# Performance work log

Hardware: AMD Instinct MI355X
Metric: run time of the kernel (lower is better)

Reference implementation:

```python
import jax, jax.numpy as jnp
import numpy as np

N_NODES = 10000
N_EDGES = 160000
B = 128
HEADS = 4
DIMS = [36, 128, 256, 512]
NEG_SLOPE = 0.2  # PyG GATConv default


def setup_inputs() -> dict:
    key = jax.random.key(0)
    ks = jax.random.split(key, 32)
    inp = {}
    inp["x"] = jax.random.normal(ks[0], (N_NODES, DIMS[0]), jnp.float32)
    inp["edge_index"] = jax.random.randint(ks[1], (2, N_EDGES), 0, N_NODES)
    inp["batch"] = jnp.sort(jax.random.randint(ks[2], (N_NODES,), 0, B))
    ki = 3
    for i in range(3):
        din, dout = DIMS[i], DIMS[i + 1]
        C = dout // HEADS
        inp[f"gcn_w{i}"] = jax.random.normal(ks[ki], (din, dout), jnp.float32) * (din ** -0.5); ki += 1
        inp[f"gcn_b{i}"] = jnp.zeros((dout,), jnp.float32)
        inp[f"gat_w{i}"] = jax.random.normal(ks[ki], (dout, dout), jnp.float32) * (dout ** -0.5); ki += 1
        inp[f"gat_as{i}"] = jax.random.normal(ks[ki], (HEADS, C), jnp.float32) * 0.1; ki += 1
        inp[f"gat_ad{i}"] = jax.random.normal(ks[ki], (HEADS, C), jnp.float32) * 0.1; ki += 1
        inp[f"gat_b{i}"] = jnp.zeros((dout,), jnp.float32)
    D = DIMS[-1]
    inp["ap_w1"] = jax.random.normal(ks[ki], (D, D // 2), jnp.float32) * (D ** -0.5); ki += 1
    inp["ap_b1"] = jnp.zeros((D // 2,), jnp.float32)
    inp["ap_w2"] = jax.random.normal(ks[ki], (D // 2, 1), jnp.float32) * ((D // 2) ** -0.5); ki += 1
    inp["ap_b2"] = jnp.zeros((1,), jnp.float32)
    return inp


def _gcn(x, w, b, src, dst, n):
    # PyG GCNConv: add self-loops, symmetric deg^-1/2 normalization, bias after agg
    h = x @ w  # [N, dout]
    deg = jax.ops.segment_sum(jnp.ones_like(dst, dtype=h.dtype), dst, n) + 1.0  # incl. self-loop
    dinv = deg ** -0.5
    norm = dinv[src] * dinv[dst]  # [E]
    agg = jax.ops.segment_sum(h[src] * norm[:, None], dst, n)
    agg = agg + h * (dinv * dinv)[:, None]  # self-loop messages
    return agg + b


def _gat(x, w, a_s, a_d, b, src, dst, n):
    # PyG GATConv: self-loops, leaky-relu logits, segment softmax over dst, concat heads
    C = w.shape[1] // HEADS
    h = (x @ w).reshape(n, HEADS, C)
    alpha_src = (h * a_s).sum(-1)  # [N, H]
    alpha_dst = (h * a_d).sum(-1)  # [N, H]
    loop = jnp.arange(n)
    s = jnp.concatenate([src, loop])
    d = jnp.concatenate([dst, loop])
    e = jax.nn.leaky_relu(alpha_src[s] + alpha_dst[d], NEG_SLOPE)  # [E+N, H]
    m = jax.ops.segment_max(e, d, n)
    ex = jnp.exp(e - m[d])
    den = jax.ops.segment_sum(ex, d, n)
    alpha = ex / den[d]  # [E+N, H]
    out = jax.ops.segment_sum(h[s] * alpha[:, :, None], d, n)  # [N, H, C]
    return out.reshape(n, HEADS * C) + b


def _forward(x, edge_index, batch, params, ap_w1, ap_b1, ap_w2, ap_b2):
    src, dst = edge_index[0], edge_index[1]
    n = x.shape[0]
    x_in = x
    n_layers = len(params)
    for i, (gw, gb, aw, a_s, a_d, ab) in enumerate(params):
        h = jax.nn.relu(_gcn(x, gw, gb, src, dst, n))  # dropout is identity in eval
        x = h + _gat(h, aw, a_s, a_d, ab, src, dst, n)
        if i < n_layers - 1:
            if x.shape[-1] == x_in.shape[-1]:
                x = x + x_in
            x_in = x
    # attention pooling (global softmax then per-graph masked renorm)
    a = jnp.tanh(x @ ap_w1 + ap_b1) @ ap_w2 + ap_b2  # [N, 1]
    a = jax.nn.softmax(a, axis=0)
    mask = jax.nn.one_hot(batch, B, dtype=x.dtype)  # [N, B]
    aw_ = a * mask
    aw_ = aw_ / (aw_.sum(0, keepdims=True) + 1e-8)
    graph_emb = aw_.T @ x  # [B, D]
    cnt = jax.ops.segment_sum(jnp.ones((n,), x.dtype), batch, B)
    ssum = jax.ops.segment_sum(x, batch, B)
    mean = ssum / jnp.maximum(cnt, 1.0)[:, None]
    smax = jax.ops.segment_max(x, batch, B)
    return jnp.concatenate([graph_emb, mean, smax, ssum], axis=1)  # [B, 4*D]


def reference(x, edge_index, batch,
              gcn_w0, gcn_b0, gat_w0, gat_as0, gat_ad0, gat_b0,
              gcn_w1, gcn_b1, gat_w1, gat_as1, gat_ad1, gat_b1,
              gcn_w2, gcn_b2, gat_w2, gat_as2, gat_ad2, gat_b2,
              ap_w1, ap_b1, ap_w2, ap_b2):
    params = [
        (gcn_w0, gcn_b0, gat_w0, gat_as0, gat_ad0, gat_b0),
        (gcn_w1, gcn_b1, gat_w1, gat_as1, gat_ad1, gat_b1),
        (gcn_w2, gcn_b2, gat_w2, gat_as2, gat_ad2, gat_b2),
    ]
    return _forward(x, edge_index, batch, params, ap_w1, ap_b1, ap_w2, ap_b2)
```

## Files before the change

### kernel.cpp

```cpp
#include <hip/hip_runtime.h>
#include <math.h>

#define NN 10000
#define NE 160000
#define NB 128
#define NH 4
#define DOUT 512
#define NEG 0.2f
#define CNT_BLKS ((NE + 255) / 256)

typedef __attribute__((ext_vector_type(8))) short short8;
typedef __attribute__((ext_vector_type(4))) float f32x4;
typedef __attribute__((ext_vector_type(4))) unsigned short us4;

__device__ __forceinline__ float leakyf(float v){ return fmaxf(v, NEG*v); }
__device__ __forceinline__ void fma4(float4& a, const float4 v, float w){
  a.x += v.x*w; a.y += v.y*w; a.z += v.z*w; a.w += v.w*w;
}
__device__ __forceinline__ unsigned short f2bf(float f){
  unsigned int u = __float_as_uint(f);
  u += 0x7FFFu + ((u >> 16) & 1u);
  return (unsigned short)(u >> 16);
}
__device__ __forceinline__ float bf2f(unsigned short h){
  return __uint_as_float(((unsigned int)h) << 16);
}
__device__ __forceinline__ void split2(float v, unsigned short& h, unsigned short& l){
  h = f2bf(v);
  l = f2bf(v - bf2f(h));
}
__device__ __forceinline__ void store_hl(unsigned short* H, unsigned short* L,
                                         size_t base, float4 v){
  us4 h, l; unsigned short hh, ll;
  split2(v.x, hh, ll); h[0]=hh; l[0]=ll;
  split2(v.y, hh, ll); h[1]=hh; l[1]=ll;
  split2(v.z, hh, ll); h[2]=hh; l[2]=ll;
  split2(v.w, hh, ll); h[3]=hh; l[3]=ll;
  *(us4*)&H[base] = h;
  *(us4*)&L[base] = l;
}
__device__ __forceinline__ void gl_lds16(const unsigned short* g, unsigned short* l){
  __builtin_amdgcn_global_load_lds(
      (const __attribute__((address_space(1))) unsigned int*)g,
      (__attribute__((address_space(3))) unsigned int*)l, 16, 0, 0);
}

struct AllConv {
  const float* src[7];
  unsigned short* dh[7];
  unsigned short* dl[7];
  int K[7], Mm[7], Kp[7], tot[7];
};

__global__ void k_count_conv(const int* __restrict__ dst, int* __restrict__ cnt,
                             AllConv a, int convTot){
  int bid = blockIdx.x;
  if (bid < CNT_BLKS){
    int e = bid*256 + threadIdx.x;
    if (e < NE) atomicAdd(&cnt[dst[e]], 1);
  } else {
    int idx = (bid - CNT_BLKS)*256 + threadIdx.x;
    if (idx >= convTot) return;
    int j = 0;
    while (idx >= a.tot[j]){ idx -= a.tot[j]; j++; }
    int Kp = a.Kp[j], K = a.K[j], M = a.Mm[j];
    int kk = idx % Kp, m = idx / Kp;
    float v = (kk < K) ? a.src[j][(size_t)kk*M + m] : 0.f;
    unsigned short h, l; split2(v, h, l);
    a.dh[j][idx] = h; a.dl[j][idx] = l;
  }
}

__global__ __launch_bounds__(1024) void k_scan_all(
    const int* __restrict__ cnt, const int* __restrict__ batch,
    int* __restrict__ rowptr, float* __restrict__ dinv,
    int* __restrict__ cursor, float* __restrict__ apre,
    int* __restrict__ starts, int* __restrict__ perm){
  __shared__ int sh[NN];
  __shared__ int pref[1024];
  __shared__ int hist[512];
  __shared__ int hbase[512];
  int t = threadIdx.x;
  for (int i = t; i < NN; i += 1024) sh[i] = cnt[i];
  if (t < 512) hist[t] = 0;
  if (t <= NB){
    int lo = 0, hi = NN;
    while (lo < hi){ int mid = (lo + hi) >> 1; if (batch[mid] < t) lo = mid + 1; else hi = mid; }
    starts[t] = lo;
  }
  __syncthreads();
  int base = t*10;
  int csum = 0;
#pragma unroll
  for (int k = 0; k < 10; k++){
    int i = base + k;
    if (i < NN){
      csum += sh[i];
      atomicAdd(&hist[511 - min(sh[i], 511)], 1);
    }
  }
  pref[t] = csum; __syncthreads();
  int horig = (t < 512) ? hist[t] : 0;
  for (int o = 1; o < 1024; o <<= 1){
    int v = (t >= o) ? pref[t - o] : 0;
    __syncthreads();
    pref[t] += v;
    __syncthreads();
  }
  for (int o = 1; o < 512; o <<= 1){
    int v = 0;
    if (t < 512 && t >= o) v = hist[t - o];
    __syncthreads();
    if (t < 512 && t >= o) hist[t] += v;
    __syncthreads();
  }
  if (t < 512) hbase[t] = hist[t] - horig;
  __syncthreads();
  int run = pref[t] - csum;
#pragma unroll
  for (int k = 0; k < 10; k++){
    int i = base + k;
    if (i < NN){
      int c = sh[i];
      rowptr[i] = run;
      run += c;
      dinv[i] = rsqrtf((float)c + 1.f);
      cursor[i] = 0;
      apre[i] = 0.f;
      int pos = atomicAdd(&hbase[511 - min(c, 511)], 1);
      perm[pos] = i;
    }
  }
  if (t == 1023) rowptr[NN] = pref[1023];
}

__global__ void k_fill(const int* __restrict__ src, const int* __restrict__ dst,
                       const int* __restrict__ rowptr, int* __restrict__ cursor,
                       int* __restrict__ colidx){
  int e = blockIdx.x*blockDim.x + threadIdx.x;
  if (e >= NE) return;
  int d = dst[e];
  int pos = atomicAdd(&cursor[d], 1);
  colidx[rowptr[d] + pos] = src[e];
}

#define GBM 64
#define GBN 128
#define GBK 64
__global__ __launch_bounds__(256) void k_gemm_bf3(
    const unsigned short* __restrict__ Ah, const unsigned short* __restrict__ Al,
    const unsigned short* __restrict__ Bh, const unsigned short* __restrict__ Bl,
    float* __restrict__ C, int N, int Kp, int M, int mode,
    const float* __restrict__ bias, unsigned short* __restrict__ outH,
    unsigned short* __restrict__ outL,
    const float* __restrict__ a_s, const float* __restrict__ a_d,
    float* __restrict__ as_o, float* __restrict__ ad_o, int Cdim){
  __shared__ unsigned short AsH[2*GBM*32], AsL[2*GBM*32];
  __shared__ unsigned short BsH[2*GBN*32], BsL[2*GBN*32];
  __shared__ float sred[2][GBM][4];
  int gx = M / GBN;
  int gy = (N + GBM - 1) / GBM;
  const int G = 8;
  int bid = blockIdx.x;
  int full = gy / G;
  int bid_full = full * G * gx;
  int by, bx;
  if (bid < bid_full){
    int g = bid / (G*gx); int rem = bid % (G*gx);
    by = g*G + rem % G; bx = rem / G;
  } else {
    int rem = bid - bid_full; int rows = gy - full*G;
    by = full*G + rem % rows; bx = rem / rows;
  }
  int row0 = by * GBM, col0 = bx * GBN;
  int t = threadIdx.x;
  int w = t >> 6, L = t & 63;
  int lm = L & 15, lq = L >> 4;
  int wc = w * 32;

  int sr = L >> 2, sc = L & 3;
  int art = w*16 + sr;
  int ga  = (sc - ((art >> 1) & 3)) & 3;
  int agrow = min(row0 + art, N-1);
  int brt0 = w*16 + sr;
  int brt1 = (w+4)*16 + sr;
  int gb0 = (sc - ((brt0 >> 1) & 3)) & 3;
  int gb1 = (sc - ((brt1 >> 1) & 3)) & 3;
  int bgrow0 = col0 + brt0, bgrow1 = col0 + brt1;

  int rc = (lq + (lm >> 1)) & 3;
  int aoff[4], boff[2];
#pragma unroll
  for (int mi = 0; mi < 4; mi++) aoff[mi] = (mi*16 + lm)*32 + rc*8;
#pragma unroll
  for (int ni = 0; ni < 2; ni++) boff[ni] = (wc + ni*16 + lm)*32 + rc*8;

  f32x4 acc[4][2];
#pragma unroll
  for (int i = 0; i < 4; i++)
#pragma unroll
    for (int j = 0; j < 2; j++) acc[i][j] = (f32x4){0.f,0.f,0.f,0.f};

  int nk = Kp / GBK;
  for (int kt = 0; kt < nk; kt++){
    int k0 = kt * GBK;
    if (kt) __syncthreads();
#pragma unroll
    for (int h = 0; h < 2; h++){
      int kh = k0 + h*32;
      gl_lds16(&Ah[(size_t)agrow*Kp + kh + ga*8],  &AsH[h*2048 + w*512]);
      gl_lds16(&Al[(size_t)agrow*Kp + kh + ga*8],  &AsL[h*2048 + w*512]);
      gl_lds16(&Bh[(size_t)bgrow0*Kp + kh + gb0*8], &BsH[h*4096 + w*512]);
      gl_lds16(&Bh[(size_t)bgrow1*Kp + kh + gb1*8], &BsH[h*4096 + (w+4)*512]);
      gl_lds16(&Bl[(size_t)bgrow0*Kp + kh + gb0*8], &BsL[h*4096 + w*512]);
      gl_lds16(&Bl[(size_t)bgrow1*Kp + kh + gb1*8], &BsL[h*4096 + (w+4)*512]);
    }
    __syncthreads();

#pragma unroll
    for (int h = 0; h < 2; h++){
      short8 ah[4], al[4], bh[2], bl[2];
#pragma unroll
      for (int mi = 0; mi < 4; mi++){
        ah[mi] = *(const short8*)&AsH[h*2048 + aoff[mi]];
        al[mi] = *(const short8*)&AsL[h*2048 + aoff[mi]];
      }
#pragma unroll
      for (int ni = 0; ni < 2; ni++){
        bh[ni] = *(const short8*)&BsH[h*4096 + boff[ni]];
        bl[ni] = *(const short8*)&BsL[h*4096 + boff[ni]];
      }
#pragma unroll
      for (int mi = 0; mi < 4; mi++)
#pragma unroll
        for (int ni = 0; ni < 2; ni++){
          acc[mi][ni] = __builtin_amdgcn_mfma_f32_16x16x32_bf16(ah[mi], bh[ni], acc[mi][ni], 0, 0, 0);
          acc[mi][ni] = __builtin_amdgcn_mfma_f32_16x16x32_bf16(ah[mi], bl[ni], acc[mi][ni], 0, 0, 0);
          acc[mi][ni] = __builtin_amdgcn_mfma_f32_16x16x32_bf16(al[mi], bh[ni], acc[mi][ni], 0, 0, 0);
        }
    }
  }
  if (mode == 1){
#pragma unroll
    for (int mi = 0; mi < 4; mi++)
#pragma unroll
      for (int ni = 0; ni < 2; ni++){
#pragma unroll
        for (int r = 0; r < 4; r++){
          int row = row0 + mi*16 + lq*4 + r;
          int col = col0 + wc + ni*16 + lm;
          if (row < N){
            float v = fmaxf(acc[mi][ni][r] + bias[col], 0.f);
            unsigned short hh, ll; split2(v, hh, ll);
            outH[(size_t)row*M + col] = hh;
            outL[(size_t)row*M + col] = ll;
            C[(size_t)row*M + col] = v;
          }
        }
      }
  } else if (mode != 3){
#pragma unroll
    for (int mi = 0; mi < 4; mi++)
#pragma unroll
      for (int ni = 0; ni < 2; ni++){
#pragma unroll
        for (int r = 0; r < 4; r++){
          int row = row0 + mi*16 + lq*4 + r;
          int col = col0 + wc + ni*16 + lm;
          if (row < N) C[(size_t)row*M + col] = acc[mi][ni][r];
        }
      }
  }
  if (mode == 2){
    float sA0 = a_s[col0 + wc + lm], sA1 = a_s[col0 + wc + 16 + lm];
    float dA0 = a_d[col0 + wc + lm], dA1 = a_d[col0 + wc + 16 + lm];
#pragma unroll
    for (int mi = 0; mi < 4; mi++)
#pragma unroll
      for (int r = 0; r < 4; r++){
        float vs = acc[mi][0][r]*sA0 + acc[mi][1][r]*sA1;
        float vd = acc[mi][0][r]*dA0 + acc[mi][1][r]*dA1;
#pragma unroll
        for (int o = 1; o <= 8; o <<= 1){
          vs += __shfl_xor(vs, o);
          vd += __shfl_xor(vd, o);
        }
        if (lm == 0){
          int row = mi*16 + lq*4 + r;
          sred[0][row][w] = vs;
          sred[1][row][w] = vd;
        }
      }
    __syncthreads();
    if (t < GBM){
      int n = row0 + t;
      if (n < N){
        int wph = Cdim >> 5;
        int nheads = 4 / wph;
        for (int g = 0; g < nheads; g++){
          float ss = 0.f, dd = 0.f;
          for (int q = 0; q < wph; q++){
            ss += sred[0][t][g*wph + q];
            dd += sred[1][t][g*wph + q];
          }
          int hd = (col0 + g*wph*32) / Cdim;
          as_o[n*NH + hd] = ss;
          ad_o[n*NH + hd] = dd;
        }
      }
    }
  } else if (mode == 3){
    float b0 = bias[col0 + wc + lm], b1v = bias[col0 + wc + 16 + lm];
    float w0v = a_s[col0 + wc + lm], w1v = a_s[col0 + wc + 16 + lm];
#pragma unroll
    for (int mi = 0; mi < 4; mi++)
#pragma unroll
      for (int r = 0; r < 4; r++){
        float v = tanhf(acc[mi][0][r] + b0)*w0v + tanhf(acc[mi][1][r] + b1v)*w1v;
#pragma unroll
        for (int o = 1; o <= 8; o <<= 1) v += __shfl_xor(v, o);
        if (lm == 0) sred[0][mi*16 + lq*4 + r][w] = v;
      }
    __syncthreads();
    if (t < GBM){
      int n = row0 + t;
      if (n < N){
        float s = sred[0][t][0] + sred[0][t][1] + sred[0][t][2] + sred[0][t][3];
        atomicAdd(&as_o[n], s);
      }
    }
  }
}

__global__ __launch_bounds__(256) void k_gcn_pre0(
    const float* __restrict__ x0, const float* __restrict__ dinv,
    const int* __restrict__ rowptr, const int* __restrict__ colidx,
    const int* __restrict__ perm,
    unsigned short* __restrict__ outH, unsigned short* __restrict__ outL){
  int t = threadIdx.x;
  int sub = t & 15;
  int gid = blockIdx.x*16 + (t >> 4);
  if (gid >= NN) return;
  int n = perm[gid];
  int f0 = sub*4;
  bool act = f0 < 36;
  int b = rowptr[n], e = rowptr[n+1];
  float dn = dinv[n];
  float4 a0 = make_float4(0,0,0,0), a1 = make_float4(0,0,0,0);
  float4 a2 = make_float4(0,0,0,0), a3 = make_float4(0,0,0,0);
  if (act){
    float4 sv = *(const float4*)&x0[(size_t)n*36 + f0];
    int j = b;
    for (; j + 7 < e; j += 8){
      int s0 = colidx[j],   s1 = colidx[j+1], s2 = colidx[j+2], s3 = colidx[j+3];
      int s4 = colidx[j+4], s5 = colidx[j+5], s6 = colidx[j+6], s7 = colidx[j+7];
      float w0 = dinv[s0], w1 = dinv[s1], w2 = dinv[s2], w3 = dinv[s3];
      float w4 = dinv[s4], w5 = dinv[s5], w6 = dinv[s6], w7 = dinv[s7];
      float4 v0 = *(const float4*)&x0[(size_t)s0*36 + f0];
      float4 v1 = *(const float4*)&x0[(size_t)s1*36 + f0];
      float4 v2 = *(const float4*)&x0[(size_t)s2*36 + f0];
      float4 v3 = *(const float4*)&x0[(size_t)s3*36 + f0];
      float4 v4 = *(const float4*)&x0[(size_t)s4*36 + f0];
      float4 v5 = *(const float4*)&x0[(size_t)s5*36 + f0];
      float4 v6 = *(const float4*)&x0[(size_t)s6*36 + f0];
      float4 v7 = *(const float4*)&x0[(size_t)s7*36 + f0];
      fma4(a0, v0, w0*dn); fma4(a1, v1, w1*dn);
      fma4(a2, v2, w2*dn); fma4(a3, v3, w3*dn);
      fma4(a0, v4, w4*dn); fma4(a1, v5, w5*dn);
      fma4(a2, v6, w6*dn); fma4(a3, v7, w7*dn);
    }
    for (; j + 3 < e; j += 4){
      int s0 = colidx[j], s1 = colidx[j+1], s2 = colidx[j+2], s3 = colidx[j+3];
      float w0 = dinv[s0], w1 = dinv[s1], w2 = dinv[s2], w3 = dinv[s3];
      float4 v0 = *(const float4*)&x0[(size_t)s0*36 + f0];
      float4 v1 = *(const float4*)&x0[(size_t)s1*36 + f0];
      float4 v2 = *(const float4*)&x0[(size_t)s2*36 + f0];
      float4 v3 = *(const float4*)&x0[(size_t)s3*36 + f0];
      fma4(a0, v0, w0*dn); fma4(a1, v1, w1*dn);
      fma4(a2, v2, w2*dn); fma4(a3, v3, w3*dn);
    }
    for (; j < e; j++){
      int s = colidx[j];
      float4 v = *(const float4*)&x0[(size_t)s*36 + f0];
      fma4(a0, v, dinv[s]*dn);
    }
    float4 acc = make_float4(a0.x+a1.x+a2.x+a3.x, a0.y+a1.y+a2.y+a3.y,
                             a0.z+a1.z+a2.z+a3.z, a0.w+a1.w+a2.w+a3.w);
    float dn2 = dn*dn;
    acc.x += sv.x*dn2; acc.y += sv.y*dn2; acc.z += sv.z*dn2; acc.w += sv.w*dn2;
    store_hl(outH, outL, (size_t)n*64 + f0, acc);
  } else {
    store_hl(outH, outL, (size_t)n*64 + f0, make_float4(0,0,0,0));
  }
}

__global__ __launch_bounds__(256) void k_gcn_pre(
    const float* __restrict__ xf, const float* __restrict__ dinv,
    const int* __restrict__ rowptr, const int* __restrict__ colidx,
    const int* __restrict__ perm,
    unsigned short* __restrict__ outH, unsigned short* __restrict__ outL,
    int Kp, int nchunk){
  int bid = blockIdx.x;
  int chunk = bid % nchunk, grp = bid / nchunk;
  int t = threadIdx.x;
  int sub = t & 15;
  int gid = grp*16 + (t >> 4);
  if (gid >= NN) return;
  int n = perm[gid];
  int f0 = chunk*64 + sub*4;
  int b = rowptr[n], e = rowptr[n+1];
  float dn = dinv[n];
  float4 sv = *(const float4*)&xf[(size_t)n*Kp + f0];
  float4 a0 = make_float4(0,0,0,0), a1 = make_float4(0,0,0,0);
  float4 a2 = make_float4(0,0,0,0), a3 = make_float4(0,0,0,0);
  int j = b;
  for (; j + 7 < e; j += 8){
    int s0 = colidx[j],   s1 = colidx[j+1], s2 = colidx[j+2], s3 = colidx[j+3];
    int s4 = colidx[j+4], s5 = colidx[j+5], s6 = colidx[j+6], s7 = colidx[j+7];
    float w0 = dinv[s0], w1 = dinv[s1], w2 = dinv[s2], w3 = dinv[s3];
    float w4 = dinv[s4], w5 = dinv[s5], w6 = dinv[s6], w7 = dinv[s7];
    float4 v0 = *(const float4*)&xf[(size_t)s0*Kp + f0];
    float4 v1 = *(const float4*)&xf[(size_t)s1*Kp + f0];
    float4 v2 = *(const float4*)&xf[(size_t)s2*Kp + f0];
    float4 v3 = *(const float4*)&xf[(size_t)s3*Kp + f0];
    float4 v4 = *(const float4*)&xf[(size_t)s4*Kp + f0];
    float4 v5 = *(const float4*)&xf[(size_t)s5*Kp + f0];
    float4 v6 = *(const float4*)&xf[(size_t)s6*Kp + f0];
    float4 v7 = *(const float4*)&xf[(size_t)s7*Kp + f0];
    fma4(a0, v0, w0*dn); fma4(a1, v1, w1*dn);
    fma4(a2, v2, w2*dn); fma4(a3, v3, w3*dn);
    fma4(a0, v4, w4*dn); fma4(a1, v5, w5*dn);
    fma4(a2, v6, w6*dn); fma4(a3, v7, w7*dn);
  }
  for (; j + 3 < e; j += 4){
    int s0 = colidx[j], s1 = colidx[j+1], s2 = colidx[j+2], s3 = colidx[j+3];
    float w0 = dinv[s0], w1 = dinv[s1], w2 = dinv[s2], w3 = dinv[s3];
    float4 v0 = *(const float4*)&xf[(size_t)s0*Kp + f0];
    float4 v1 = *(const float4*)&xf[(size_t)s1*Kp + f0];
    float4 v2 = *(const float4*)&xf[(size_t)s2*Kp + f0];
    float4 v3 = *(const float4*)&xf[(size_t)s3*Kp + f0];
    fma4(a0, v0, w0*dn); fma4(a1, v1, w1*dn);
    fma4(a2, v2, w2*dn); fma4(a3, v3, w3*dn);
  }
  for (; j < e; j++){
    int s = colidx[j];
    float4 v = *(const float4*)&xf[(size_t)s*Kp + f0];
    fma4(a0, v, dinv[s]*dn);
  }
  float4 acc = make_float4(a0.x+a1.x+a2.x+a3.x, a0.y+a1.y+a2.y+a3.y,
                           a0.z+a1.z+a2.z+a3.z, a0.w+a1.w+a2.w+a3.w);
  float dn2 = dn*dn;
  acc.x += sv.x*dn2; acc.y += sv.y*dn2; acc.z += sv.z*dn2; acc.w += sv.w*dn2;
  store_hl(outH, outL, (size_t)n*Kp + f0, acc);
}

__global__ __launch_bounds__(256) void k_gat_gather(
    const float* __restrict__ hg, const float* __restrict__ hf,
    const int* __restrict__ rowptr, const int* __restrict__ colidx,
    const int* __restrict__ perm,
    const float* __restrict__ as_, const float* __restrict__ ad_,
    const float* __restrict__ ab,
    unsigned short* __restrict__ outH, unsigned short* __restrict__ outL,
    float* __restrict__ xf,
    int M, int C, int nchunk){
  int bid = blockIdx.x;
  int chunk = bid % nchunk, grp = bid / nchunk;
  int t = threadIdx.x;
  int sub = t & 15;
  int gid = grp*16 + (t >> 4);
  if (gid >= NN) return;
  int n = perm[gid];
  int f0 = chunk*64 + sub*4;
  int hd = f0 / C;
  int b = rowptr[n], e = rowptr[n+1];
  int ai = n*NH + hd;
  float adn = ad_[ai];
  float sl = fminf(fmaxf(leakyf(as_[ai] + adn), -80.f), 80.f);
  float es = __expf(sl);
  float4 sv = *(const float4*)&hg[(size_t)n*M + f0];
  float4 hv = *(const float4*)&hf[(size_t)n*M + f0];
  float4 bb = *(const float4*)&ab[f0];
  float d = es;
  float4 a0 = make_float4(0,0,0,0), a1 = make_float4(0,0,0,0);
  float4 a2 = make_float4(0,0,0,0), a3 = make_float4(0,0,0,0);
  int j = b;
  for (; j + 7 < e; j += 8){
    int s0 = colidx[j],   s1 = colidx[j+1], s2 = colidx[j+2], s3 = colidx[j+3];
    int s4 = colidx[j+4], s5 = colidx[j+5], s6 = colidx[j+6], s7 = colidx[j+7];
    float l0 = leakyf(as_[s0*NH + hd] + adn), l1 = leakyf(as_[s1*NH + hd] + adn);
    float l2 = leakyf(as_[s2*NH + hd] + adn), l3 = leakyf(as_[s3*NH + hd] + adn);
    float l4 = leakyf(as_[s4*NH + hd] + adn), l5 = leakyf(as_[s5*NH + hd] + adn);
    float l6 = leakyf(as_[s6*NH + hd] + adn), l7 = leakyf(as_[s7*NH + hd] + adn);
    float4 v0 = *(const float4*)&hg[(size_t)s0*M + f0];
    float4 v1 = *(const float4*)&hg[(size_t)s1*M + f0];
    float4 v2 = *(const float4*)&hg[(size_t)s2*M + f0];
    float4 v3 = *(const float4*)&hg[(size_t)s3*M + f0];
    float4 v4 = *(const float4*)&hg[(size_t)s4*M + f0];
    float4 v5 = *(const float4*)&hg[(size_t)s5*M + f0];
    float4 v6 = *(const float4*)&hg[(size_t)s6*M + f0];
    float4 v7 = *(const float4*)&hg[(size_t)s7*M + f0];
    float w0 = __expf(fminf(fmaxf(l0,-80.f),80.f)), w1 = __expf(fminf(fmaxf(l1,-80.f),80.f));
    float w2 = __expf(fminf(fmaxf(l2,-80.f),80.f)), w3 = __expf(fminf(fmaxf(l3,-80.f),80.f));
    float w4 = __expf(fminf(fmaxf(l4,-80.f),80.f)), w5 = __expf(fminf(fmaxf(l5,-80.f),80.f));
    float w6 = __expf(fminf(fmaxf(l6,-80.f),80.f)), w7 = __expf(fminf(fmaxf(l7,-80.f),80.f));
    d += ((w0 + w1) + (w2 + w3)) + ((w4 + w5) + (w6 + w7));
    fma4(a0, v0, w0); fma4(a1, v1, w1);
    fma4(a2, v2, w2); fma4(a3, v3, w3);
    fma4(a0, v4, w4); fma4(a1, v5, w5);
    fma4(a2, v6, w6); fma4(a3, v7, w7);
  }
  for (; j < e; j++){
    int s = colidx[j];
    float l = leakyf(as_[s*NH + hd] + adn);
    float4 v = *(const float4*)&hg[(size_t)s*M + f0];
    float ww = __expf(fminf(fmaxf(l,-80.f),80.f));
    d += ww;
    fma4(a0, v, ww);
  }
  float4 acc = make_float4(a0.x+a1.x+a2.x+a3.x, a0.y+a1.y+a2.y+a3.y,
                           a0.z+a1.z+a2.z+a3.z, a0.w+a1.w+a2.w+a3.w);
  float inv = 1.f/d;
  float4 r = make_float4(
    hv.x + bb.x + (sv.x*es + acc.x)*inv,
    hv.y + bb.y + (sv.y*es + acc.y)*inv,
    hv.z + bb.z + (sv.z*es + acc.z)*inv,
    hv.w + bb.w + (sv.w*es + acc.w)*inv);
  *(float4*)&xf[(size_t)n*M + f0] = r;
  store_hl(outH, outL, (size_t)n*M + f0, r);
}

__global__ __launch_bounds__(512) void k_pool(
    const float* __restrict__ xf,
    const float* __restrict__ apre, const int* __restrict__ starts,
    float* __restrict__ out){
  __shared__ float red[512];
  __shared__ float4 comb[3][8][64];
  int g = blockIdx.x >> 1, half = blockIdx.x & 1;
  int t = threadIdx.x;
  int b = starts[g], e = starts[g+1];
  float m = -INFINITY;
  for (int n = b + t; n < e; n += 512) m = fmaxf(m, apre[n]);
  red[t] = m; __syncthreads();
  for (int o = 256; o > 0; o >>= 1){
    if (t < o) red[t] = fmaxf(red[t], red[t + o]);
    __syncthreads();
  }
  m = red[0]; __syncthreads();
  float s = 0.f;
  for (int n = b + t; n < e; n += 512) s += __expf(apre[n] - m);
  red[t] = s; __syncthreads();
  for (int o = 256; o > 0; o >>= 1){
    if (t < o) red[t] += red[t + o];
    __syncthreads();
  }
  float inv = 1.f / (red[0] + 1e-8f);
  int lf = t & 63, sl = t >> 6;
  int fo = half*64 + lf;
  float4 sum = make_float4(0,0,0,0), wacc = make_float4(0,0,0,0);
  float4 mx = make_float4(-INFINITY,-INFINITY,-INFINITY,-INFINITY);
  for (int n = b + sl; n < e; n += 8){
    float4 xv = *(const float4*)&xf[(size_t)n*DOUT + fo*4];
    float p = __expf(apre[n] - m) * inv;
    sum.x += xv.x; sum.y += xv.y; sum.z += xv.z; sum.w += xv.w;
    mx.x = fmaxf(mx.x, xv.x); mx.y = fmaxf(mx.y, xv.y);
    mx.z = fmaxf(mx.z, xv.z); mx.w = fmaxf(mx.w, xv.w);
    fma4(wacc, xv, p);
  }
  comb[0][sl][lf] = wacc; comb[1][sl][lf] = sum; comb[2][sl][lf] = mx;
  __syncthreads();
  if (sl == 0){
#pragma unroll
    for (int q = 1; q < 8; q++){
      float4 w2 = comb[0][q][lf], s2 = comb[1][q][lf], m2 = comb[2][q][lf];
      wacc.x += w2.x; wacc.y += w2.y; wacc.z += w2.z; wacc.w += w2.w;
      sum.x += s2.x; sum.y += s2.y; sum.z += s2.z; sum.w += s2.w;
      mx.x = fmaxf(mx.x, m2.x); mx.y = fmaxf(mx.y, m2.y);
      mx.z = fmaxf(mx.z, m2.z); mx.w = fmaxf(mx.w, m2.w);
    }
    float ic = 1.f / fmaxf((float)(e - b), 1.f);
    float4* o = (float4*)(out + (size_t)g*4*DOUT);
    o[fo]       = wacc;
    o[128 + fo] = make_float4(sum.x*ic, sum.y*ic, sum.z*ic, sum.w*ic);
    o[256 + fo] = mx;
    o[384 + fo] = sum;
  }
}

extern "C" void kernel_launch(void* const* d_in, const int* in_sizes, int n_in,
                              void* d_out, int out_size, void* d_ws, size_t ws_size,
                              hipStream_t stream) {
  const float* x0   = (const float*)d_in[0];
  const int*   ei   = (const int*)d_in[1];
  const int*   src  = ei;
  const int*   dst  = ei + NE;
  const int*   batch= (const int*)d_in[2];
  const float* gw[3]  = {(const float*)d_in[3],  (const float*)d_in[9],  (const float*)d_in[15]};
  const float* gb[3]  = {(const float*)d_in[4],  (const float*)d_in[10], (const float*)d_in[16]};
  const float* aw[3]  = {(const float*)d_in[5],  (const float*)d_in[11], (const float*)d_in[17]};
  const float* asw[3] = {(const float*)d_in[6],  (const float*)d_in[12], (const float*)d_in[18]};
  const float* adw[3] = {(const float*)d_in[7],  (const float*)d_in[13], (const float*)d_in[19]};
  const float* ab[3]  = {(const float*)d_in[8],  (const float*)d_in[14], (const float*)d_in[20]};
  const float* apw1 = (const float*)d_in[21];
  const float* apb1 = (const float*)d_in[22];
  const float* apw2 = (const float*)d_in[23];
  float* out = (float*)d_out;

  char* p = (char*)d_ws;
  auto alloc = [&](size_t bytes) -> void* {
    void* r = (void*)p; p += (bytes + 255) & ~(size_t)255; return r;
  };
  float* f1 = (float*)alloc((size_t)NN*512*4);
  float* hf = (float*)alloc((size_t)NN*512*4);
  float* xf = (float*)alloc((size_t)NN*512*4);
  unsigned short* actH0 = (unsigned short*)alloc((size_t)NN*512*2);
  unsigned short* actL0 = (unsigned short*)alloc((size_t)NN*512*2);
  unsigned short* actH1 = (unsigned short*)alloc((size_t)NN*512*2);
  unsigned short* actL1 = (unsigned short*)alloc((size_t)NN*512*2);
  unsigned short* preH  = (unsigned short*)alloc((size_t)NN*256*2);
  unsigned short* preL  = (unsigned short*)alloc((size_t)NN*256*2);
  const int wK[7]  = {36, 128, 128, 256, 256, 512, 512};
  const int wM[7]  = {128, 128, 256, 256, 512, 512, 256};
  const int wKp[7] = {64, 128, 128, 256, 256, 512, 512};
  const float* wsrc[7] = {gw[0], aw[0], gw[1], aw[1], gw[2], aw[2], apw1};
  unsigned short* wTh[7]; unsigned short* wTl[7];
  for (int i = 0; i < 7; i++){
    size_t sz = (size_t)wM[i]*wKp[i]*2;
    wTh[i] = (unsigned short*)alloc(sz);
    wTl[i] = (unsigned short*)alloc(sz);
  }
  float* dinv = (float*)alloc(NN*4);
  float* as_  = (float*)alloc(NN*NH*4);
  float* ad_  = (float*)alloc(NN*NH*4);
  float* apre = (float*)alloc(NN*4);
  int* rowptr = (int*)alloc((NN+1)*4);
  int* colidx = (int*)alloc((size_t)NE*4);
  int* cnt    = (int*)alloc(NN*4);
  int* cursor = (int*)alloc(NN*4);
  int* starts = (int*)alloc((NB+1)*4);
  int* perm   = (int*)alloc(NN*4);

  AllConv ac;
  int convTot = 0;
  for (int i = 0; i < 7; i++){
    ac.src[i] = wsrc[i]; ac.dh[i] = wTh[i]; ac.dl[i] = wTl[i];
    ac.K[i] = wK[i]; ac.Mm[i] = wM[i]; ac.Kp[i] = wKp[i];
    ac.tot[i] = wKp[i]*wM[i];
    convTot += ac.tot[i];
  }

  hipMemsetAsync(cnt, 0, NN*sizeof(int), stream);
  int convBlks = (convTot + 255) / 256;
  k_count_conv<<<CNT_BLKS + convBlks, 256, 0, stream>>>(dst, cnt, ac, convTot);
  k_scan_all<<<1, 1024, 0, stream>>>(cnt, batch, rowptr, dinv, cursor, apre, starts, perm);
  k_fill<<<(NE+255)/256, 256, 0, stream>>>(src, dst, rowptr, cursor, colidx);

  const int dims[4] = {36, 128, 256, 512};
  const int ngrp = (NN + 15) / 16;
  int wi = 0;
  for (int i = 0; i < 3; i++){
    int Kin = (i == 0) ? 64 : dims[i];
    int M = dims[i+1], C = M/NH;
    int nchunk_in = Kin / 64;
    int nchunk = M / 64;
    int nblk = (M/GBN) * ((NN+GBM-1)/GBM);
    if (i == 0){
      k_gcn_pre0<<<ngrp, 256, 0, stream>>>(x0, dinv, rowptr, colidx, perm, preH, preL);
    } else {
      k_gcn_pre<<<nchunk_in*ngrp, 256, 0, stream>>>(xf, dinv, rowptr, colidx, perm,
                                                    preH, preL, Kin, nchunk_in);
    }
    k_gemm_bf3<<<nblk, 256, 0, stream>>>(preH, preL, wTh[wi], wTl[wi], hf, NN, wKp[wi], M,
                                         1, gb[i], actH0, actL0,
                                         nullptr, nullptr, nullptr, nullptr, C);
    wi++;
    k_gemm_bf3<<<nblk, 256, 0, stream>>>(actH0, actL0, wTh[wi], wTl[wi], f1, NN, wKp[wi], M,
                                         2, nullptr, nullptr, nullptr,
                                         asw[i], adw[i], as_, ad_, C);
    wi++;
    k_gat_gather<<<nchunk*ngrp, 256, 0, stream>>>(f1, hf, rowptr, colidx, perm,
                                                  as_, ad_, ab[i],
                                                  actH1, actL1, xf, M, C, nchunk);
  }

  {
    int nblk = (256/GBN) * ((NN+GBM-1)/GBM);
    k_gemm_bf3<<<nblk, 256, 0, stream>>>(actH1, actL1, wTh[6], wTl[6], nullptr, NN, wKp[6], 256,
                                         3, apb1, nullptr, nullptr,
                                         apw2, nullptr, apre, nullptr, 64);
  }
  k_pool<<<NB*2, 512, 0, stream>>>(xf, apre, starts, out);
}
```

Before: 376.6 us.

## Fuse degree counting into scan and pooling into final GEMM epilogue

Degree counting moves into the single-block scan kernel using LDS atomics, which removes a memset and a separate launch. CSR fill and weight conversion merge into one launch. The pooling kernel is removed: the last block of the attention-score GEMM to finish each graph, tracked with a global completion counter, computes that graph's softmax pooling, mean, max and sum. This saves launches, but it serializes the pooling onto a few tail blocks with less parallelism and makes the single-block scan do all 160k edge atomics.

New measurement: 443.7 us. 1.18x slower.

```diff
diff --git a/kernel.cpp b/kernel.cpp
--- a/kernel.cpp
+++ b/kernel.cpp
@@ -52,42 +52,26 @@
   int K[7], Mm[7], Kp[7], tot[7];
 };
 
-__global__ void k_count_conv(const int* __restrict__ dst, int* __restrict__ cnt,
-                             AllConv a, int convTot){
-  int bid = blockIdx.x;
-  if (bid < CNT_BLKS){
-    int e = bid*256 + threadIdx.x;
-    if (e < NE) atomicAdd(&cnt[dst[e]], 1);
-  } else {
-    int idx = (bid - CNT_BLKS)*256 + threadIdx.x;
-    if (idx >= convTot) return;
-    int j = 0;
-    while (idx >= a.tot[j]){ idx -= a.tot[j]; j++; }
-    int Kp = a.Kp[j], K = a.K[j], M = a.Mm[j];
-    int kk = idx % Kp, m = idx / Kp;
-    float v = (kk < K) ? a.src[j][(size_t)kk*M + m] : 0.f;
-    unsigned short h, l; split2(v, h, l);
-    a.dh[j][idx] = h; a.dl[j][idx] = l;
-  }
-}
-
 __global__ __launch_bounds__(1024) void k_scan_all(
-    const int* __restrict__ cnt, const int* __restrict__ batch,
+    const int* __restrict__ dst, const int* __restrict__ batch,
     int* __restrict__ rowptr, float* __restrict__ dinv,
     int* __restrict__ cursor, float* __restrict__ apre,
-    int* __restrict__ starts, int* __restrict__ perm){
+    int* __restrict__ starts, int* __restrict__ perm,
+    int* __restrict__ gexp, int* __restrict__ gdone, float* __restrict__ outp){
   __shared__ int sh[NN];
   __shared__ int pref[1024];
   __shared__ int hist[512];
   __shared__ int hbase[512];
   int t = threadIdx.x;
-  for (int i = t; i < NN; i += 1024) sh[i] = cnt[i];
+  for (int i = t; i < NN; i += 1024) sh[i] = 0;
   if (t < 512) hist[t] = 0;
   if (t <= NB){
     int lo = 0, hi = NN;
     while (lo < hi){ int mid = (lo + hi) >> 1; if (batch[mid] < t) lo = mid + 1; else hi = mid; }
     starts[t] = lo;
   }
+  __syncthreads();
+  for (int i = t; i < NE; i += 1024) atomicAdd(&sh[dst[i]], 1);
   __syncthreads();
   int base = t*10;
   int csum = 0;
@@ -132,16 +116,42 @@
     }
   }
   if (t == 1023) rowptr[NN] = pref[1023];
-}
-
-__global__ void k_fill(const int* __restrict__ src, const int* __restrict__ dst,
-                       const int* __restrict__ rowptr, int* __restrict__ cursor,
-                       int* __restrict__ colidx){
-  int e = blockIdx.x*blockDim.x + threadIdx.x;
-  if (e >= NE) return;
-  int d = dst[e];
-  int pos = atomicAdd(&cursor[d], 1);
-  colidx[rowptr[d] + pos] = src[e];
+  __syncthreads();
+  if (t < NB){
+    int b0 = starts[t], e0 = starts[t+1];
+    gdone[t] = 0;
+    gexp[t] = (e0 > b0) ? 2*(((e0-1) >> 6) - (b0 >> 6) + 1) : 0x7fffffff;
+    if (e0 == b0){
+      float4* o = (float4*)(outp + (size_t)t*4*DOUT);
+      float4 z = make_float4(0.f,0.f,0.f,0.f);
+      float4 ni = make_float4(-INFINITY,-INFINITY,-INFINITY,-INFINITY);
+      for (int q = 0; q < 128; q++){ o[q]=z; o[128+q]=z; o[256+q]=ni; o[384+q]=z; }
+    }
+  }
+}
+
+__global__ void k_fill_conv(const int* __restrict__ src, const int* __restrict__ dst,
+                            const int* __restrict__ rowptr, int* __restrict__ cursor,
+                            int* __restrict__ colidx, AllConv a, int convTot){
+  int bid = blockIdx.x;
+  if (bid < CNT_BLKS){
+    int e = bid*256 + threadIdx.x;
+    if (e < NE){
+      int d = dst[e];
+      int pos = atomicAdd(&cursor[d], 1);
+      colidx[rowptr[d] + pos] = src[e];
+    }
+  } else {
+    int idx = (bid - CNT_BLKS)*256 + threadIdx.x;
+    if (idx >= convTot) return;
+    int j = 0;
+    while (idx >= a.tot[j]){ idx -= a.tot[j]; j++; }
+    int Kp = a.Kp[j], K = a.K[j], M = a.Mm[j];
+    int kk = idx % Kp, m = idx / Kp;
+    float v = (kk < K) ? a.src[j][(size_t)kk*M + m] : 0.f;
+    unsigned short h, l; split2(v, h, l);
+    a.dh[j][idx] = h; a.dl[j][idx] = l;
+  }
 }
 
 #define GBM 64
@@ -154,10 +164,15 @@
     const float* __restrict__ bias, unsigned short* __restrict__ outH,
     unsigned short* __restrict__ outL,
     const float* __restrict__ a_s, const float* __restrict__ a_d,
-    float* __restrict__ as_o, float* __restrict__ ad_o, int Cdim){
+    float* __restrict__ as_o, float* __restrict__ ad_o, int Cdim,
+    const int* __restrict__ starts, const int* __restrict__ gexp,
+    int* __restrict__ gdone, const float* __restrict__ xfull,
+    float* __restrict__ outp){
   __shared__ unsigned short AsH[2*GBM*32], AsL[2*GBM*32];
   __shared__ unsigned short BsH[2*GBN*32], BsL[2*GBN*32];
   __shared__ float sred[2][GBM][4];
+  __shared__ int winners[8];
+  __shared__ int nwin;
   int gx = M / GBN;
   int gy = (N + GBM - 1) / GBM;
   const int G = 8;
@@ -328,6 +343,77 @@
         float s = sred[0][t][0] + sred[0][t][1] + sred[0][t][2] + sred[0][t][3];
         atomicAdd(&as_o[n], s);
       }
+    }
+    __syncthreads();
+    __threadfence();
+    if (t == 0){
+      nwin = 0;
+      int row1 = min(row0 + GBM, N);
+      int glo = NB, ghi = -1;
+      { int a2 = 0, b2 = NB-1;
+        while (a2 <= b2){ int m2 = (a2+b2)>>1; if (starts[m2+1] > row0){ glo = m2; b2 = m2-1; } else a2 = m2+1; } }
+      { int a2 = 0, b2 = NB-1;
+        while (a2 <= b2){ int m2 = (a2+b2)>>1; if (starts[m2] < row1){ ghi = m2; a2 = m2+1; } else b2 = m2-1; } }
+      for (int g = glo; g <= ghi && g < NB; g++){
+        if (starts[g+1] > starts[g]){
+          int old = atomicAdd(&gdone[g], 1);
+          if (old == gexp[g]-1 && nwin < 8) winners[nwin++] = g;
+        }
+      }
+    }
+    __syncthreads();
+    int nw = nwin;
+    for (int wix = 0; wix < nw; wix++){
+      int g = winners[wix];
+      int gb = starts[g], ge = starts[g+1];
+      float* red = (float*)AsH;
+      float4* comb = (float4*)BsH;
+      float m = -INFINITY;
+      for (int n = gb + t; n < ge; n += 256) m = fmaxf(m, as_o[n]);
+      red[t] = m; __syncthreads();
+      for (int o2 = 128; o2 > 0; o2 >>= 1){
+        if (t < o2) red[t] = fmaxf(red[t], red[t + o2]);
+        __syncthreads();
+      }
+      m = red[0]; __syncthreads();
+      float s = 0.f;
+      for (int n = gb + t; n < ge; n += 256) s += __expf(as_o[n] - m);
+      red[t] = s; __syncthreads();
+      for (int o2 = 128; o2 > 0; o2 >>= 1){
+        if (t < o2) red[t] += red[t + o2];
+        __syncthreads();
+      }
+      float inv = 1.f / (red[0] + 1e-8f);
+      __syncthreads();
+      int lf = t & 127, sl2 = t >> 7;
+      float4 sum = make_float4(0,0,0,0), wacc = make_float4(0,0,0,0);
+      float4 mx = make_float4(-INFINITY,-INFINITY,-INFINITY,-INFINITY);
+      for (int n = gb + sl2; n < ge; n += 2){
+        float4 xv = *(const float4*)&xfull[(size_t)n*DOUT + lf*4];
+        float pw = __expf(as_o[n] - m) * inv;
+        sum.x += xv.x; sum.y += xv.y; sum.z += xv.z; sum.w += xv.w;
+        mx.x = fmaxf(mx.x, xv.x); mx.y = fmaxf(mx.y, xv.y);
+        mx.z = fmaxf(mx.z, xv.z); mx.w = fmaxf(mx.w, xv.w);
+        fma4(wacc, xv, pw);
+      }
+      comb[(0*2 + sl2)*128 + lf] = wacc;
+      comb[(1*2 + sl2)*128 + lf] = sum;
+      comb[(2*2 + sl2)*128 + lf] = mx;
+      __syncthreads();
+      if (sl2 == 0){
+        float4 w2 = comb[(0*2+1)*128+lf], s2 = comb[(1*2+1)*128+lf], m2 = comb[(2*2+1)*128+lf];
+        wacc.x += w2.x; wacc.y += w2.y; wacc.z += w2.z; wacc.w += w2.w;
+        sum.x += s2.x; sum.y += s2.y; sum.z += s2.z; sum.w += s2.w;
+        mx.x = fmaxf(mx.x, m2.x); mx.y = fmaxf(mx.y, m2.y);
+        mx.z = fmaxf(mx.z, m2.z); mx.w = fmaxf(mx.w, m2.w);
+        float ic = 1.f / fmaxf((float)(ge - gb), 1.f);
+        float4* o = (float4*)(outp + (size_t)g*4*DOUT);
+        o[lf]       = wacc;
+        o[128 + lf] = make_float4(sum.x*ic, sum.y*ic, sum.z*ic, sum.w*ic);
+        o[256 + lf] = mx;
+        o[384 + lf] = sum;
+      }
+      __syncthreads();
     }
   }
 }
@@ -529,63 +615,6 @@
   store_hl(outH, outL, (size_t)n*M + f0, r);
 }
 
-__global__ __launch_bounds__(512) void k_pool(
-    const float* __restrict__ xf,
-    const float* __restrict__ apre, const int* __restrict__ starts,
-    float* __restrict__ out){
-  __shared__ float red[512];
-  __shared__ float4 comb[3][8][64];
-  int g = blockIdx.x >> 1, half = blockIdx.x & 1;
-  int t = threadIdx.x;
-  int b = starts[g], e = starts[g+1];
-  float m = -INFINITY;
-  for (int n = b + t; n < e; n += 512) m = fmaxf(m, apre[n]);
-  red[t] = m; __syncthreads();
-  for (int o = 256; o > 0; o >>= 1){
-    if (t < o) red[t] = fmaxf(red[t], red[t + o]);
-    __syncthreads();
-  }
-  m = red[0]; __syncthreads();
-  float s = 0.f;
-  for (int n = b + t; n < e; n += 512) s += __expf(apre[n] - m);
-  red[t] = s; __syncthreads();
-  for (int o = 256; o > 0; o >>= 1){
-    if (t < o) red[t] += red[t + o];
-    __syncthreads();
-  }
-  float inv = 1.f / (red[0] + 1e-8f);
-  int lf = t & 63, sl = t >> 6;
-  int fo = half*64 + lf;
-  float4 sum = make_float4(0,0,0,0), wacc = make_float4(0,0,0,0);
-  float4 mx = make_float4(-INFINITY,-INFINITY,-INFINITY,-INFINITY);
-  for (int n = b + sl; n < e; n += 8){
-    float4 xv = *(const float4*)&xf[(size_t)n*DOUT + fo*4];
-    float p = __expf(apre[n] - m) * inv;
-    sum.x += xv.x; sum.y += xv.y; sum.z += xv.z; sum.w += xv.w;
-    mx.x = fmaxf(mx.x, xv.x); mx.y = fmaxf(mx.y, xv.y);
-    mx.z = fmaxf(mx.z, xv.z); mx.w = fmaxf(mx.w, xv.w);
-    fma4(wacc, xv, p);
-  }
-  comb[0][sl][lf] = wacc; comb[1][sl][lf] = sum; comb[2][sl][lf] = mx;
-  __syncthreads();
-  if (sl == 0){
-#pragma unroll
-    for (int q = 1; q < 8; q++){
-      float4 w2 = comb[0][q][lf], s2 = comb[1][q][lf], m2 = comb[2][q][lf];
-      wacc.x += w2.x; wacc.y += w2.y; wacc.z += w2.z; wacc.w += w2.w;
-      sum.x += s2.x; sum.y += s2.y; sum.z += s2.z; sum.w += s2.w;
-      mx.x = fmaxf(mx.x, m2.x); mx.y = fmaxf(mx.y, m2.y);
-      mx.z = fmaxf(mx.z, m2.z); mx.w = fmaxf(mx.w, m2.w);
-    }
-    float ic = 1.f / fmaxf((float)(e - b), 1.f);
-    float4* o = (float4*)(out + (size_t)g*4*DOUT);
-    o[fo]       = wacc;
-    o[128 + fo] = make_float4(sum.x*ic, sum.y*ic, sum.z*ic, sum.w*ic);
-    o[256 + fo] = mx;
-    o[384 + fo] = sum;
-  }
-}
-
 extern "C" void kernel_launch(void* const* d_in, const int* in_sizes, int n_in,
                               void* d_out, int out_size, void* d_ws, size_t ws_size,
                               hipStream_t stream) {
@@ -634,10 +663,11 @@
   float* apre = (float*)alloc(NN*4);
   int* rowptr = (int*)alloc((NN+1)*4);
   int* colidx = (int*)alloc((size_t)NE*4);
-  int* cnt    = (int*)alloc(NN*4);
   int* cursor = (int*)alloc(NN*4);
   int* starts = (int*)alloc((NB+1)*4);
   int* perm   = (int*)alloc(NN*4);
+  int* gexp   = (int*)alloc(NB*4);
+  int* gdone  = (int*)alloc(NB*4);
 
   AllConv ac;
   int convTot = 0;
@@ -648,11 +678,11 @@
     convTot += ac.tot[i];
   }
 
-  hipMemsetAsync(cnt, 0, NN*sizeof(int), stream);
+  k_scan_all<<<1, 1024, 0, stream>>>(dst, batch, rowptr, dinv, cursor, apre,
+                                     starts, perm, gexp, gdone, out);
   int convBlks = (convTot + 255) / 256;
-  k_count_conv<<<CNT_BLKS + convBlks, 256, 0, stream>>>(dst, cnt, ac, convTot);
-  k_scan_all<<<1, 1024, 0, stream>>>(cnt, batch, rowptr, dinv, cursor, apre, starts, perm);
-  k_fill<<<(NE+255)/256, 256, 0, stream>>>(src, dst, rowptr, cursor, colidx);
+  k_fill_conv<<<CNT_BLKS + convBlks, 256, 0, stream>>>(src, dst, rowptr, cursor,
+                                                       colidx, ac, convTot);
 
   const int dims[4] = {36, 128, 256, 512};
   const int ngrp = (NN + 15) / 16;
@@ -671,11 +701,13 @@
     }
     k_gemm_bf3<<<nblk, 256, 0, stream>>>(preH, preL, wTh[wi], wTl[wi], hf, NN, wKp[wi], M,
                                          1, gb[i], actH0, actL0,
-                                         nullptr, nullptr, nullptr, nullptr, C);
+                                         nullptr, nullptr, nullptr, nullptr, C,
+                                         nullptr, nullptr, nullptr, nullptr, nullptr);
     wi++;
     k_gemm_bf3<<<nblk, 256, 0, stream>>>(actH0, actL0, wTh[wi], wTl[wi], f1, NN, wKp[wi], M,
                                          2, nullptr, nullptr, nullptr,
-                                         asw[i], adw[i], as_, ad_, C);
+                                         asw[i], adw[i], as_, ad_, C,
+                                         nullptr, nullptr, nullptr, nullptr, nullptr);
     wi++;
     k_gat_gather<<<nchunk*ngrp, 256, 0, stream>>>(f1, hf, rowptr, colidx, perm,
                                                   as_, ad_, ab[i],
@@ -686,7 +718,7 @@
     int nblk = (256/GBN) * ((NN+GBM-1)/GBM);
     k_gemm_bf3<<<nblk, 256, 0, stream>>>(actH1, actL1, wTh[6], wTl[6], nullptr, NN, wKp[6], 256,
                                          3, apb1, nullptr, nullptr,
-                                         apw2, nullptr, apre, nullptr, 64);
-  }
-  k_pool<<<NB*2, 512, 0, stream>>>(xf, apre, starts, out);
-}
+                                         apw2, nullptr, apre, nullptr, 64,
+                                         starts, gexp, gdone, xf, out);
+  }
+}
```
